# Kernel optimization log

Hardware: AMD Instinct MI355X
Metric: run time of the kernel (lower is better)

## Reference

```python
import jax, jax.numpy as jnp
import numpy as np

# dims
B, L, HID, TDIM, LT = 8, 4096, 1024, 768, 77
DIM = 512            # vmamba_dim
D_INNER = 2 * DIM    # expand = 2
NHEADS = DIM // 16   # 32
HEADDIM = D_INNER // NHEADS  # 32
D_STATE = 64
CONV_K = 4
CONV_DIM = D_INNER + 2 * D_STATE  # 1152
D_PROJ = 2 * D_INNER + 2 * D_STATE + NHEADS  # z | xBC | dt


def setup_inputs() -> dict:
    key = jax.random.key(0)
    ks = jax.random.split(key, 20)
    s = 0.02
    return {
        "image_tokens": jax.random.normal(ks[0], (B, L, HID), jnp.float32),
        "text_tokens": jax.random.normal(ks[1], (B, LT, TDIM), jnp.float32),
        "W_in": jax.random.normal(ks[2], (HID, DIM), jnp.float32) * s,
        "b_in": jnp.zeros((DIM,), jnp.float32),
        "W_txt": jax.random.normal(ks[3], (TDIM, DIM), jnp.float32) * s,
        "b_txt": jnp.zeros((DIM,), jnp.float32),
        "norm_w": jnp.ones((DIM,), jnp.float32),
        "norm_b": jnp.zeros((DIM,), jnp.float32),
        "W_zxbcdt": jax.random.normal(ks[4], (DIM, D_PROJ), jnp.float32) * s,
        "b_zxbcdt": jnp.zeros((D_PROJ,), jnp.float32),
        "conv_w": jax.random.normal(ks[5], (CONV_DIM, CONV_K), jnp.float32) * 0.1,
        "conv_b": jnp.zeros((CONV_DIM,), jnp.float32),
        "dt_bias": jax.random.uniform(ks[6], (NHEADS,), jnp.float32, -4.0, -2.0),
        "A_log": jnp.log(jnp.arange(1, NHEADS + 1, dtype=jnp.float32)),
        "D": jnp.ones((NHEADS,), jnp.float32),
        "W_blk_out": jax.random.normal(ks[7], (D_INNER, DIM), jnp.float32) * s,
        "b_blk_out": jnp.zeros((DIM,), jnp.float32),
        "W_out": jax.random.normal(ks[8], (DIM, HID), jnp.float32) * s,
        "b_out": jnp.zeros((HID,), jnp.float32),
    }


def _layernorm(x, w, b, eps=1e-5):
    mu = x.mean(-1, keepdims=True)
    var = ((x - mu) ** 2).mean(-1, keepdims=True)
    return (x - mu) * jax.lax.rsqrt(var + eps) * w + b


def _mamba2_block(tok, norm_w, norm_b, W_zxbcdt, b_zxbcdt, conv_w, conv_b,
                  dt_bias, A_log, Dp, W_blk_out, b_blk_out):
    x = _layernorm(tok, norm_w, norm_b)
    zxbcdt = x @ W_zxbcdt + b_zxbcdt                       # [B,L,D_PROJ]
    z = zxbcdt[..., :D_INNER]
    xBC = zxbcdt[..., D_INNER:D_INNER + CONV_DIM]
    dt = zxbcdt[..., D_INNER + CONV_DIM:]                  # [B,L,H]
    # causal depthwise conv1d, kernel 4
    xp = jnp.pad(xBC, ((0, 0), (CONV_K - 1, 0), (0, 0)))
    conv = sum(xp[:, k:k + L, :] * conv_w[None, None, :, k] for k in range(CONV_K))
    xBC = jax.nn.silu(conv + conv_b)
    xh = xBC[..., :D_INNER].reshape(B, L, NHEADS, HEADDIM)  # [B,L,H,P]
    Bm = xBC[..., D_INNER:D_INNER + D_STATE]                # [B,L,N]
    Cm = xBC[..., D_INNER + D_STATE:]                       # [B,L,N]
    dt = jax.nn.softplus(dt + dt_bias)                      # [B,L,H]
    A = -jnp.exp(A_log)                                     # [H]
    dA = jnp.exp(dt * A)                                    # [B,L,H]

    def step(h, xs):
        dA_t, dt_t, B_t, C_t, x_t = xs   # [B,H],[B,H],[B,N],[B,N],[B,H,P]
        h = h * dA_t[:, :, None, None] + \
            (dt_t[:, :, None, None] * x_t[..., None]) * B_t[:, None, None, :]
        y = jnp.einsum('bhpn,bn->bhp', h, C_t)
        return h, y

    xs = (dA.transpose(1, 0, 2), dt.transpose(1, 0, 2),
          Bm.transpose(1, 0, 2), Cm.transpose(1, 0, 2),
          xh.transpose(1, 0, 2, 3))
    h0 = jnp.zeros((B, NHEADS, HEADDIM, D_STATE), tok.dtype)
    _, ys = jax.lax.scan(step, h0, xs)                      # [L,B,H,P]
    y = ys.transpose(1, 0, 2, 3) + Dp[None, None, :, None] * xh
    y = y.reshape(B, L, D_INNER) * jax.nn.silu(z)
    return tok + (y @ W_blk_out + b_blk_out)                # residual


def reference(image_tokens, text_tokens, W_in, b_in, W_txt, b_txt,
              norm_w, norm_b, W_zxbcdt, b_zxbcdt, conv_w, conv_b,
              dt_bias, A_log, D, W_blk_out, b_blk_out, W_out, b_out):
    txt = text_tokens[:, 0, :] @ W_txt + b_txt              # cls pool
    tok = image_tokens @ W_in + b_in + txt[:, None, :]
    tok = _mamba2_block(tok, norm_w, norm_b, W_zxbcdt, b_zxbcdt, conv_w,
                        conv_b, dt_bias, A_log, D, W_blk_out, b_blk_out)
    tok = tok @ W_out + b_out                               # [B,L,HID]
    return tok.mean(axis=1)                                 # AdaptiveAvgPool1d(1)
```

## Files before the change

### kernel.cpp

```cpp
#include <hip/hip_runtime.h>

typedef unsigned short U16;
typedef __attribute__((ext_vector_type(2))) float f32x2;
typedef __attribute__((ext_vector_type(4))) float f32x4;
typedef __attribute__((ext_vector_type(8))) short short8;
typedef __attribute__((ext_vector_type(8))) __bf16 bf16x8;

#define Bsz 8
#define Lsz 4096
#define HID 1024
#define DIMV 512
#define D_INNER 1024
#define NHEADS 32
#define HEADDIM 32
#define D_STATE 64
#define CONV_DIM 1152
#define D_PROJ 2208
#define D_PROJ_PAD 2304
#define MROWS 32768
#define CL2 256
#define NSUB 4
#define NCH 16

__device__ __forceinline__ float bf2f(U16 u) {
  return __builtin_bit_cast(float, (unsigned)(((unsigned)u) << 16));
}
__device__ __forceinline__ U16 f2bf(float f) {
  unsigned u = __builtin_bit_cast(unsigned, f);
  return (U16)((u + 0x7FFFu + ((u >> 16) & 1u)) >> 16);
}
__device__ __forceinline__ void gload_lds16(const void* g, void* l) {
  __builtin_amdgcn_global_load_lds((const __attribute__((address_space(1))) unsigned int*)g,
                                   (__attribute__((address_space(3))) unsigned int*)l, 16, 0, 0);
}

__global__ __launch_bounds__(512) void txt_kernel(const float* __restrict__ text,
                                                  const float* __restrict__ Wt,
                                                  const float* __restrict__ bt,
                                                  float* __restrict__ txt) {
  int b = blockIdx.x, j = threadIdx.x;
  float s = bt[j];
  const float* tp = text + (size_t)b * 77 * 768;
  for (int k = 0; k < 768; ++k) s += tp[k] * Wt[(size_t)k * 512 + j];
  txt[b * 512 + j] = s;
}

__global__ __launch_bounds__(256) void transpose_cvt_kernel(const float* __restrict__ in,
                                                            U16* __restrict__ out,
                                                            int K, int N, int Npad) {
  __shared__ U16 tile[32][33];
  int n0 = blockIdx.x * 32, k0 = blockIdx.y * 32;
  int tx = threadIdx.x, ty = threadIdx.y;
  #pragma unroll
  for (int i = 0; i < 4; ++i) {
    int k = k0 + ty + i * 8, n = n0 + tx;
    float v = (n < N) ? in[(size_t)k * N + n] : 0.f;
    tile[ty + i * 8][tx] = f2bf(v);
  }
  __syncthreads();
  #pragma unroll
  for (int i = 0; i < 4; ++i) {
    int n = n0 + ty + i * 8;
    out[(size_t)n * K + k0 + tx] = tile[tx][ty + i * 8];
  }
}

template <int EPI, int AF32>
__global__ __launch_bounds__(256) void gemm_kernel(const void* __restrict__ Ap,
                                                   const U16* __restrict__ Bt,
                                                   U16* __restrict__ C,
                                                   const float* __restrict__ bias,
                                                   const float* __restrict__ txtv,
                                                   int M, int K, int Nreal) {
  __shared__ alignas(16) U16 As[128 * 64];
  __shared__ alignas(16) U16 Bs[128 * 64];
  const int tid = threadIdx.x;
  const int wid = tid >> 6, lane = tid & 63;
  const int lhi = lane >> 4, llo = lane & 15;
  const int m0 = blockIdx.x * 128;
  const int n0 = blockIdx.y * 128;
  const int wr = wid >> 1, wc = wid & 1;
  f32x4 acc[4][4] = {};

  for (int k0 = 0; k0 < K; k0 += 64) {
    __syncthreads();
    if constexpr (AF32) {
      const float* Af = (const float*)Ap;
      #pragma unroll
      for (int is = 0; is < 4; ++is) {
        int q = is * 256 + tid;
        int r = q >> 3, cl = q & 7;
        int cg = cl ^ (r & 7);
        const float* src = Af + (size_t)(m0 + r) * K + k0 + cg * 8;
        f32x4 v0 = *reinterpret_cast<const f32x4*>(src);
        f32x4 v1 = *reinterpret_cast<const f32x4*>(src + 4);
        short8 o;
        #pragma unroll
        for (int j = 0; j < 4; ++j) {
          o[j] = (short)f2bf(v0[j]);
          o[j + 4] = (short)f2bf(v1[j]);
        }
        *reinterpret_cast<short8*>(&As[q * 8]) = o;
      }
    } else {
      const U16* A = (const U16*)Ap;
      #pragma unroll
      for (int is = 0; is < 4; ++is) {
        int qbase = is * 256 + wid * 64;
        int q = qbase + lane;
        int r = q >> 3;
        int cc = (q & 7) ^ (r & 7);
        gload_lds16(A + (size_t)(m0 + r) * K + k0 + cc * 8, &As[qbase * 8]);
      }
    }
    #pragma unroll
    for (int is = 0; is < 4; ++is) {
      int qbase = is * 256 + wid * 64;
      int q = qbase + lane;
      int r = q >> 3;
      int cc = (q & 7) ^ (r & 7);
      gload_lds16(Bt + (size_t)(n0 + r) * K + k0 + cc * 8, &Bs[qbase * 8]);
    }
    __syncthreads();
    #pragma unroll
    for (int kk = 0; kk < 64; kk += 32) {
      bf16x8 av[4], bv[4];
      #pragma unroll
      for (int i = 0; i < 4; ++i) {
        int ra = wr * 64 + i * 16 + llo;
        short8 a = *reinterpret_cast<const short8*>(
            &As[ra * 64 + ((((kk >> 3) + lhi) ^ (ra & 7)) << 3)]);
        av[i] = __builtin_bit_cast(bf16x8, a);
        int rb = wc * 64 + i * 16 + llo;
        short8 b = *reinterpret_cast<const short8*>(
            &Bs[rb * 64 + ((((kk >> 3) + lhi) ^ (rb & 7)) << 3)]);
        bv[i] = __builtin_bit_cast(bf16x8, b);
      }
      #pragma unroll
      for (int i = 0; i < 4; ++i)
        #pragma unroll
        for (int j = 0; j < 4; ++j)
          acc[i][j] = __builtin_amdgcn_mfma_f32_16x16x32_bf16(av[i], bv[j], acc[i][j], 0, 0, 0);
    }
  }
  const int b = m0 >> 12;
  #pragma unroll
  for (int i = 0; i < 4; ++i) {
    int rbase = m0 + wr * 64 + i * 16 + lhi * 4;
    #pragma unroll
    for (int j = 0; j < 4; ++j) {
      int cg = n0 + wc * 64 + j * 16 + llo;
      if (cg < Nreal) {
        float badd = bias[cg] + (EPI ? txtv[b * 512 + cg] : 0.f);
        #pragma unroll
        for (int r = 0; r < 4; ++r)
          C[(size_t)(rbase + r) * Nreal + cg] = f2bf(acc[i][j][r] + badd);
      }
    }
  }
}

__global__ __launch_bounds__(128) void ln_kernel(const U16* __restrict__ tok,
                                                 U16* __restrict__ xo,
                                                 const float* __restrict__ w,
                                                 const float* __restrict__ bb) {
  int row = blockIdx.x, tid = threadIdx.x;
  const U16* rp = tok + (size_t)row * 512 + tid * 4;
  uint2 raw = *reinterpret_cast<const uint2*>(rp);
  float f0 = bf2f((U16)(raw.x & 0xffff)), f1 = bf2f((U16)(raw.x >> 16));
  float f2 = bf2f((U16)(raw.y & 0xffff)), f3 = bf2f((U16)(raw.y >> 16));
  float s = f0 + f1 + f2 + f3;
  float q = f0 * f0 + f1 * f1 + f2 * f2 + f3 * f3;
  for (int m = 1; m < 64; m <<= 1) { s += __shfl_xor(s, m); q += __shfl_xor(q, m); }
  __shared__ float ss[2], qq[2];
  if ((tid & 63) == 0) { ss[tid >> 6] = s; qq[tid >> 6] = q; }
  __syncthreads();
  s = ss[0] + ss[1]; q = qq[0] + qq[1];
  float mu = s * (1.f / 512.f);
  float var = q * (1.f / 512.f) - mu * mu;
  float rs = rsqrtf(var + 1e-5f);
  int j0 = tid * 4;
  unsigned c0 = f2bf((f0 - mu) * rs * w[j0] + bb[j0]);
  unsigned c1 = f2bf((f1 - mu) * rs * w[j0 + 1] + bb[j0 + 1]);
  unsigned c2 = f2bf((f2 - mu) * rs * w[j0 + 2] + bb[j0 + 2]);
  unsigned c3 = f2bf((f3 - mu) * rs * w[j0 + 3] + bb[j0 + 3]);
  uint2 o; o.x = c0 | (c1 << 16); o.y = c2 | (c3 << 16);
  *reinterpret_cast<uint2*>(xo + (size_t)row * 512 + j0) = o;
}

__global__ __launch_bounds__(256) void tokpart_kernel(const U16* __restrict__ tok,
                                                      float* __restrict__ part) {
  int b = blockIdx.x, j = blockIdx.y * 256 + threadIdx.x, z = blockIdx.z;
  float s = 0.f;
  int l0 = z * 256;
  for (int l = l0; l < l0 + 256; ++l)
    s += bf2f(tok[((size_t)b * Lsz + l) * 512 + j]);
  part[(z * 8 + b) * 512 + j] = s;
}

__global__ __launch_bounds__(256) void decay_kernel(const U16* __restrict__ zx,
                                                    const float* __restrict__ dt_bias,
                                                    const float* __restrict__ A_log,
                                                    float* __restrict__ decay4) {
  const int sc = blockIdx.x;
  const int w = threadIdx.x >> 6, l = threadIdx.x & 63;
  const int r0 = sc * 64;
  const int b = r0 >> 12, l0 = r0 & 4095;
  #pragma unroll
  for (int i = 0; i < 8; ++i) {
    int hh = w * 8 + i;
    float raw = bf2f(zx[(size_t)(r0 + l) * D_PROJ + 2176 + hh]) + dt_bias[hh];
    float dt = (raw > 20.f) ? raw : log1pf(__expf(raw));
    float A = -__expf(A_log[hh]);
    float ldA2 = dt * A * 1.44269504088896f;
    float ldt2 = __log2f(dt);
    float la = ldA2;
    #pragma unroll
    for (int d = 1; d < 64; d <<= 1) {
      float o = __shfl_up(la, d);
      if (l >= d) la += o;
    }
    float laend = __shfl(la, 63);
    f32x4 v = {ldt2 - la, la, exp2f(la), exp2f(laend + ldt2 - la)};
    *reinterpret_cast<f32x4*>(decay4 + ((size_t)(b * 32 + hh) * 4096 + l0 + l) * 4) = v;
  }
}

__global__ __launch_bounds__(256) void conv_tr_kernel(
    const U16* __restrict__ zx, const float* __restrict__ cw,
    const float* __restrict__ cb, U16* __restrict__ Bmo, U16* __restrict__ Cmo,
    U16* __restrict__ xh_t, U16* __restrict__ gz_t,
    U16* __restrict__ bm_t, U16* __restrict__ cm_t) {
  __shared__ U16 tile[64 * 72];
  const int lt = blockIdx.x, ct = blockIdx.y;
  const int r0 = lt * 64;
  const int b = r0 >> 12, l0 = r0 & 4095;
  const int tid = threadIdx.x;
  const int c = tid & 63, lqb = tid >> 6;

  if (ct < 16) {
    const int zc0 = ct * 64;
    #pragma unroll
    for (int it = 0; it < 4; ++it) {
      int lq4 = (lqb + it * 4) * 4;
      float v[4];
      #pragma unroll
      for (int j = 0; j < 4; ++j) {
        float z = bf2f(zx[(size_t)(r0 + lq4 + j) * D_PROJ + zc0 + c]);
        v[j] = z / (1.f + __expf(-z));
      }
      uint2 p2;
      p2.x = (unsigned)f2bf(v[0]) | ((unsigned)f2bf(v[1]) << 16);
      p2.y = (unsigned)f2bf(v[2]) | ((unsigned)f2bf(v[3]) << 16);
      *reinterpret_cast<uint2*>(reinterpret_cast<char*>(tile) + (size_t)c * 144 + lq4 * 2) = p2;
    }
    __syncthreads();
    int c2 = tid >> 2, seg = tid & 3;
    const char* src = reinterpret_cast<const char*>(tile) + (size_t)c2 * 144 + seg * 32;
    f32x4 a = *reinterpret_cast<const f32x4*>(src);
    f32x4 bq = *reinterpret_cast<const f32x4*>(src + 16);
    U16* dst = gz_t + ((size_t)b * 1024 + zc0 + c2) * 4096 + l0 + seg * 16;
    *reinterpret_cast<f32x4*>(dst) = a;
    *reinterpret_cast<f32x4*>(dst + 8) = bq;
  } else {
    const int cc = (ct - 16) * 64 + c;
    const float4 w4 = *reinterpret_cast<const float4*>(cw + cc * 4);
    const float cbv = cb[cc];
    #pragma unroll
    for (int it = 0; it < 4; ++it) {
      int lq4 = (lqb + it * 4) * 4;
      float v7[7];
      #pragma unroll
      for (int k = 0; k < 7; ++k) {
        int lrel = lq4 + k - 3;
        v7[k] = (l0 + lrel >= 0)
                    ? bf2f(zx[(size_t)(r0 + lrel) * D_PROJ + D_INNER + cc])
                    : 0.f;
      }
      float o[4];
      #pragma unroll
      for (int j = 0; j < 4; ++j) {
        float acc = cbv + v7[j] * w4.x + v7[j + 1] * w4.y + v7[j + 2] * w4.z + v7[j + 3] * w4.w;
        o[j] = acc / (1.f + __expf(-acc));
      }
      uint2 p2;
      p2.x = (unsigned)f2bf(o[0]) | ((unsigned)f2bf(o[1]) << 16);
      p2.y = (unsigned)f2bf(o[2]) | ((unsigned)f2bf(o[3]) << 16);
      *reinterpret_cast<uint2*>(reinterpret_cast<char*>(tile) + (size_t)c * 144 + lq4 * 2) = p2;
      if (cc >= 1024) {
        U16* outp = (cc < 1088) ? Bmo : Cmo;
        int n = cc & 63;
        #pragma unroll
        for (int j = 0; j < 4; ++j)
          outp[(size_t)(r0 + lq4 + j) * 64 + n] = f2bf(o[j]);
      }
    }
    __syncthreads();
    int c2 = tid >> 2, seg = tid & 3;
    const char* src = reinterpret_cast<const char*>(tile) + (size_t)c2 * 144 + seg * 32;
    f32x4 a = *reinterpret_cast<const f32x4*>(src);
    f32x4 bq = *reinterpret_cast<const f32x4*>(src + 16);
    int cc2 = (ct - 16) * 64 + c2;
    U16* dst;
    if (cc2 < 1024)      dst = xh_t + ((size_t)b * 1024 + cc2) * 4096 + l0 + seg * 16;
    else if (cc2 < 1088) dst = bm_t + ((size_t)(b * 64 + cc2 - 1024)) * 4096 + l0 + seg * 16;
    else                 dst = cm_t + ((size_t)(b * 64 + cc2 - 1088)) * 4096 + l0 + seg * 16;
    *reinterpret_cast<f32x4*>(dst) = a;
    *reinterpret_cast<f32x4*>(dst + 8) = bq;
  }
}

__global__ __launch_bounds__(256, 2) void scan_chunk_kernel(
    const U16* __restrict__ xh_t, const U16* __restrict__ gz_t,
    const U16* __restrict__ Bm, const U16* __restrict__ Cm,
    const U16* __restrict__ bm_t, const U16* __restrict__ cm_t,
    const float* __restrict__ decay4, const float* __restrict__ Dp,
    U16* __restrict__ hpart, U16* __restrict__ wacc,
    float* __restrict__ ylocal, float* __restrict__ aprod) {
  const int w = threadIdx.x >> 6, l = threadIdx.x & 63;
  const int bid = (blockIdx.x & 7) * 128 + (blockIdx.x >> 3);
  const int u = bid * 4 + w;
  const int hh = u & 31, ci = (u >> 5) & (NCH - 1), b = u >> 9;
  const int tl = l & 15, lg = l >> 4;

  __shared__ alignas(16) U16 MsmAll[4 * 64 * 72];
  __shared__ alignas(16) float decAll[4 * 256];
  U16* Msm = &MsmAll[w * 64 * 72];
  float* qsm = &decAll[w * 256];
  float* la2sm = qsm + 64;
  float* casm = qsm + 128;
  float* cfsm = qsm + 192;

  #pragma unroll
  for (int i = 0; i < 9; ++i)
    *reinterpret_cast<f32x4*>(reinterpret_cast<char*>(Msm) + (size_t)l * 144 + i * 16) =
        f32x4{0.f, 0.f, 0.f, 0.f};

  f32x4 hC[2][4] = {};
  f32x4 WB[2][4] = {};
  f32x4 corrp[2] = {};
  float ylac[2] = {0.f, 0.f}, dxac[2] = {0.f, 0.f};
  float capfx = 1.f;
  const size_t xgrow = ((size_t)b * 1024 + hh * 32) * 4096;
  const float* dbase = decay4 + ((size_t)(b * 32 + hh) * 4096) * 4;

  for (int sc = 0; sc < NSUB; ++sc) {
    const int lglob = ci * CL2 + sc * 64;
    const int r0g = b * 4096 + lglob;

    f32x4 dv = *reinterpret_cast<const f32x4*>(dbase + (size_t)(lglob + l) * 4);
    qsm[l] = dv[0];
    la2sm[l] = dv[1];
    casm[l] = dv[2];
    cfsm[l] = dv[3];
    const float cs = __shfl(dv[2], 63);

    {
      f32x4 g[7] = {};
      #pragma unroll
      for (int k = 0; k < 2; ++k) {
        bf16x8 af0 = *reinterpret_cast<const bf16x8*>(
            Bm + (size_t)(r0g + tl) * 64 + k * 32 + lg * 8);
        bf16x8 af1 = *reinterpret_cast<const bf16x8*>(
            Bm + (size_t)(r0g + 16 + tl) * 64 + k * 32 + lg * 8);
        #pragma unroll
        for (int ti = 0; ti < 4; ++ti) {
          bf16x8 cf = *reinterpret_cast<const bf16x8*>(
              Cm + (size_t)(r0g + ti * 16 + tl) * 64 + k * 32 + lg * 8);
          g[ti] = __builtin_amdgcn_mfma_f32_16x16x32_bf16(af0, cf, g[ti], 0, 0, 0);
          if (ti >= 1)
            g[3 + ti] = __builtin_amdgcn_mfma_f32_16x16x32_bf16(af1, cf, g[3 + ti], 0, 0, 0);
        }
      }
      f32x4 q0 = *reinterpret_cast<const f32x4*>(&qsm[lg * 4]);
      f32x4 q1 = *reinterpret_cast<const f32x4*>(&qsm[16 + lg * 4]);
      #pragma unroll
      for (int idx = 0; idx < 7; ++idx) {
        const int si = (idx < 4) ? 0 : 1;
        const int ti = (idx < 4) ? idx : (idx - 3);
        f32x4 q4 = si ? q1 : q0;
        float lat = la2sm[ti * 16 + tl];
        float v[4];
        #pragma unroll
        for (int r = 0; r < 4; ++r) {
          float val = g[idx][r] * exp2f(lat + q4[r]);
          if (si == ti) val = (lg * 4 + r <= tl) ? val : 0.f;
          v[r] = val;
        }
        uint2 pk;
        pk.x = (unsigned)f2bf(v[0]) | ((unsigned)f2bf(v[1]) << 16);
        pk.y = (unsigned)f2bf(v[2]) | ((unsigned)f2bf(v[3]) << 16);
        *reinterpret_cast<uint2*>(reinterpret_cast<char*>(Msm) +
                                  (size_t)(ti * 16 + tl) * 144 + (size_t)(si * 16 + lg * 4) * 2) = pk;
      }
    }
    {
      f32x4 g[3] = {};
      #pragma unroll
      for (int k = 0; k < 2; ++k) {
        bf16x8 af2 = *reinterpret_cast<const bf16x8*>(
            Bm + (size_t)(r0g + 32 + tl) * 64 + k * 32 + lg * 8);
        bf16x8 af3 = *reinterpret_cast<const bf16x8*>(
            Bm + (size_t)(r0g + 48 + tl) * 64 + k * 32 + lg * 8);
        bf16x8 cf2 = *reinterpret_cast<const bf16x8*>(
            Cm + (size_t)(r0g + 32 + tl) * 64 + k * 32 + lg * 8);
        bf16x8 cf3 = *reinterpret_cast<const bf16x8*>(
            Cm + (size_t)(r0g + 48 + tl) * 64 + k * 32 + lg * 8);
        g[0] = __builtin_amdgcn_mfma_f32_16x16x32_bf16(af2, cf2, g[0], 0, 0, 0);
        g[1] = __builtin_amdgcn_mfma_f32_16x16x32_bf16(af2, cf3, g[1], 0, 0, 0);
        g[2] = __builtin_amdgcn_mfma_f32_16x16x32_bf16(af3, cf3, g[2], 0, 0, 0);
      }
      f32x4 q2 = *reinterpret_cast<const f32x4*>(&qsm[32 + lg * 4]);
      f32x4 q3 = *reinterpret_cast<const f32x4*>(&qsm[48 + lg * 4]);
      const int sis[3] = {2, 2, 3};
      const int tis[3] = {2, 3, 3};
      #pragma unroll
      for (int idx = 0; idx < 3; ++idx) {
        const int si = sis[idx], ti = tis[idx];
        f32x4 q4 = (si == 2) ? q2 : q3;
        float lat = la2sm[ti * 16 + tl];
        float v[4];
        #pragma unroll
        for (int r = 0; r < 4; ++r) {
          float val = g[idx][r] * exp2f(lat + q4[r]);
          if (si == ti) val = (lg * 4 + r <= tl) ? val : 0.f;
          v[r] = val;
        }
        uint2 pk;
        pk.x = (unsigned)f2bf(v[0]) | ((unsigned)f2bf(v[1]) << 16);
        pk.y = (unsigned)f2bf(v[2]) | ((unsigned)f2bf(v[3]) << 16);
        *reinterpret_cast<uint2*>(reinterpret_cast<char*>(Msm) +
                                  (size_t)(ti * 16 + tl) * 144 + (size_t)(si * 16 + lg * 4) * 2) = pk;
      }
    }

    {
      bf16x8 xb[2][2];
      #pragma unroll
      for (int pt = 0; pt < 2; ++pt)
        #pragma unroll
        for (int ks = 0; ks < 2; ++ks)
          xb[pt][ks] = *reinterpret_cast<const bf16x8*>(
              xh_t + xgrow + (size_t)(pt * 16 + tl) * 4096 + lglob + ks * 32 + lg * 8);
      #pragma unroll
      for (int tt = 0; tt < 4; ++tt) {
        f32x4 y[2] = {f32x4{0.f, 0.f, 0.f, 0.f}, f32x4{0.f, 0.f, 0.f, 0.f}};
        #pragma unroll
        for (int ks = 0; ks < 2; ++ks) {
          bf16x8 mf = *reinterpret_cast<const bf16x8*>(
              reinterpret_cast<char*>(Msm) + (size_t)(tt * 16 + tl) * 144 + (ks * 32 + lg * 8) * 2);
          #pragma unroll
          for (int pt = 0; pt < 2; ++pt)
            y[pt] = __builtin_amdgcn_mfma_f32_16x16x32_bf16(mf, xb[pt][ks], y[pt], 0, 0, 0);
        }
        #pragma unroll
        for (int pt = 0; pt < 2; ++pt) {
          size_t ro = xgrow + (size_t)(pt * 16 + tl) * 4096 + lglob + tt * 16 + lg * 4;
          uint2 gz2 = *reinterpret_cast<const uint2*>(gz_t + ro);
          uint2 xx2 = *reinterpret_cast<const uint2*>(xh_t + ro);
          float gzv[4] = {bf2f((U16)(gz2.x & 0xffff)), bf2f((U16)(gz2.x >> 16)),
                          bf2f((U16)(gz2.y & 0xffff)), bf2f((U16)(gz2.y >> 16))};
          float xxv[4] = {bf2f((U16)(xx2.x & 0xffff)), bf2f((U16)(xx2.x >> 16)),
                          bf2f((U16)(xx2.y & 0xffff)), bf2f((U16)(xx2.y >> 16))};
          #pragma unroll
          for (int r = 0; r < 4; ++r) {
            ylac[pt] = fmaf(gzv[r], y[pt][r], ylac[pt]);
            dxac[pt] = fmaf(gzv[r], xxv[r], dxac[pt]);
          }
        }
      }
    }

    bf16x8 ga[2][2], xa[2][2];
    #pragma unroll
    for (int pt = 0; pt < 2; ++pt)
      #pragma unroll
      for (int kt = 0; kt < 2; ++kt) {
        size_t ro = xgrow + (size_t)(pt * 16 + tl) * 4096 + lglob + kt * 32 + lg * 8;
        short8 graw = *reinterpret_cast<const short8*>(gz_t + ro);
        short8 xraw = *reinterpret_cast<const short8*>(xh_t + ro);
        const float* cap = &casm[kt * 32 + lg * 8];
        const float* cfp = &cfsm[kt * 32 + lg * 8];
        short8 gs, xs8;
        #pragma unroll
        for (int j = 0; j < 8; ++j) {
          gs[j] = (short)f2bf(bf2f((U16)graw[j]) * cap[j]);
          xs8[j] = (short)f2bf(bf2f((U16)xraw[j]) * cfp[j]);
        }
        ga[pt][kt] = __builtin_bit_cast(bf16x8, gs);
        xa[pt][kt] = __builtin_bit_cast(bf16x8, xs8);
      }

    #pragma unroll
    for (int nt = 0; nt < 4; ++nt) {
      size_t cro = (size_t)(b * 64 + nt * 16 + tl) * 4096 + lglob;
      bf16x8 cb0 = *reinterpret_cast<const bf16x8*>(cm_t + cro + lg * 8);
      bf16x8 cb1 = *reinterpret_cast<const bf16x8*>(cm_t + cro + 32 + lg * 8);
      bf16x8 bb0 = *reinterpret_cast<const bf16x8*>(bm_t + cro + lg * 8);
      bf16x8 bb1 = *reinterpret_cast<const bf16x8*>(bm_t + cro + 32 + lg * 8);
      #pragma unroll
      for (int pt = 0; pt < 2; ++pt) {
        f32x4 z4 = {0.f, 0.f, 0.f, 0.f};
        f32x4 ws = __builtin_amdgcn_mfma_f32_16x16x32_bf16(ga[pt][0], cb0, z4, 0, 0, 0);
        ws = __builtin_amdgcn_mfma_f32_16x16x32_bf16(ga[pt][1], cb1, ws, 0, 0, 0);
        f32x4 hs = __builtin_amdgcn_mfma_f32_16x16x32_bf16(xa[pt][0], bb0, z4, 0, 0, 0);
        hs = __builtin_amdgcn_mfma_f32_16x16x32_bf16(xa[pt][1], bb1, hs, 0, 0, 0);
        corrp[pt] = corrp[pt] + hC[pt][nt] * ws;
        WB[pt][nt] = WB[pt][nt] + ws * capfx;
        hC[pt][nt] = hC[pt][nt] * cs + hs;
      }
    }
    capfx *= cs;
  }

  #pragma unroll
  for (int pt = 0; pt < 2; ++pt)
    #pragma unroll
    for (int nt = 0; nt < 4; ++nt) {
      size_t slot = (size_t)u * 2048 + (size_t)((pt * 4 + nt) * 64 + l) * 4;
      ushort4 hp, wp;
      hp.x = f2bf(hC[pt][nt][0]); hp.y = f2bf(hC[pt][nt][1]);
      hp.z = f2bf(hC[pt][nt][2]); hp.w = f2bf(hC[pt][nt][3]);
      wp.x = f2bf(WB[pt][nt][0]); wp.y = f2bf(WB[pt][nt][1]);
      wp.z = f2bf(WB[pt][nt][2]); wp.w = f2bf(WB[pt][nt][3]);
      *reinterpret_cast<ushort4*>(hpart + slot) = hp;
      *reinterpret_cast<ushort4*>(wacc + slot) = wp;
    }
  float corrv[2][4];
  #pragma unroll
  for (int pt = 0; pt < 2; ++pt)
    #pragma unroll
    for (int r = 0; r < 4; ++r) {
      float c = corrp[pt][r];
      c += __shfl_xor(c, 1); c += __shfl_xor(c, 2);
      c += __shfl_xor(c, 4); c += __shfl_xor(c, 8);
      corrv[pt][r] = c;
    }
  const float Dh = Dp[hh];
  float* ysm = qsm;
  #pragma unroll
  for (int pt = 0; pt < 2; ++pt) {
    float yv = ylac[pt] + Dh * dxac[pt];
    yv += __shfl_xor(yv, 16);
    yv += __shfl_xor(yv, 32);
    if (l < 16) ysm[pt * 16 + l] = yv;
  }
  if (tl == 0) {
    #pragma unroll
    for (int pt = 0; pt < 2; ++pt)
      #pragma unroll
      for (int r = 0; r < 4; ++r)
        ysm[pt * 16 + lg * 4 + r] += corrv[pt][r];
  }
  if (l < 32) ylocal[(size_t)u * 32 + l] = ysm[l];
  if (l == 0) aprod[u] = capfx;
}

__global__ __launch_bounds__(256) void scan_combine_kernel(
    const U16* __restrict__ hpart, const U16* __restrict__ wacc,
    const float* __restrict__ ylocal, const float* __restrict__ aprod,
    float* __restrict__ yysum) {
  const int bh = blockIdx.x;
  const int b = bh >> 5, hh = bh & 31;
  const int w = threadIdx.x >> 6, l = threadIdx.x & 63;
  const int tl = l & 15, lg = l >> 4;
  __shared__ float csm[8][16];
  __shared__ float ylsm[32];
  const int pair0 = w * 2;
  f32x4 hr[2] = {};
  float cv[2][4] = {};
  for (int ci = 0; ci < NCH; ++ci) {
    int bx = (b * NCH + ci) * 32 + hh;
    size_t base = (size_t)bx * 2048 + (size_t)l * 4;
    float ap = aprod[bx];
    #pragma unroll
    for (int k = 0; k < 2; ++k) {
      size_t o = base + (size_t)(pair0 + k) * 256;
      ushort4 wraw = *reinterpret_cast<const ushort4*>(wacc + o);
      ushort4 praw = *reinterpret_cast<const ushort4*>(hpart + o);
      f32x4 wv = {bf2f(wraw.x), bf2f(wraw.y), bf2f(wraw.z), bf2f(wraw.w)};
      f32x4 pv = {bf2f(praw.x), bf2f(praw.y), bf2f(praw.z), bf2f(praw.w)};
      f32x4 a4 = hr[k] * wv;
      #pragma unroll
      for (int r = 0; r < 4; ++r) cv[k][r] += a4[r];
      hr[k] = hr[k] * ap + pv;
    }
  }
  #pragma unroll
  for (int k = 0; k < 2; ++k)
    #pragma unroll
    for (int r = 0; r < 4; ++r) {
      float c = cv[k][r];
      c += __shfl_xor(c, 1); c += __shfl_xor(c, 2);
      c += __shfl_xor(c, 4); c += __shfl_xor(c, 8);
      if (tl == 0) csm[pair0 + k][lg * 4 + r] = c;
    }
  if (threadIdx.x < 32) {
    float yl = 0.f;
    for (int ci = 0; ci < NCH; ++ci)
      yl += ylocal[(size_t)((b * NCH + ci) * 32 + hh) * 32 + threadIdx.x];
    ylsm[threadIdx.x] = yl;
  }
  __syncthreads();
  if (threadIdx.x < 32) {
    int p = threadIdx.x;
    int pt = p >> 4, pl = p & 15;
    float corr = csm[pt * 4 + 0][pl] + csm[pt * 4 + 1][pl] +
                 csm[pt * 4 + 2][pl] + csm[pt * 4 + 3][pl];
    yysum[(size_t)b * 1024 + hh * 32 + p] = ylsm[p] + corr;
  }
}

__global__ __launch_bounds__(128) void final1_kernel(const float* __restrict__ tokpart,
                                                     const float* __restrict__ yysum,
                                                     const float* __restrict__ Wb,
                                                     const float* __restrict__ bb,
                                                     float* __restrict__ m2) {
  int b = blockIdx.x, j = blockIdx.y * 128 + threadIdx.x;
  float tm = 0.f;
  #pragma unroll
  for (int z = 0; z < 16; ++z) tm += tokpart[(z * 8 + b) * 512 + j];
  float s = 0.f;
  for (int d = 0; d < 1024; ++d) s += yysum[b * 1024 + d] * Wb[(size_t)d * 512 + j];
  m2[b * 512 + j] = (tm + s) * (1.f / (float)Lsz) + bb[j];
}

__global__ __launch_bounds__(256) void final2_kernel(const float* __restrict__ m2,
                                                     const float* __restrict__ Wo,
                                                     const float* __restrict__ bo,
                                                     float* __restrict__ out) {
  int b = blockIdx.x, o = blockIdx.y * 256 + threadIdx.x;
  float s = 0.f;
  for (int j = 0; j < 512; ++j) s += m2[b * 512 + j] * Wo[(size_t)j * 1024 + o];
  out[b * 1024 + o] = s + bo[o];
}

extern "C" void kernel_launch(void* const* d_in, const int* in_sizes, int n_in,
                              void* d_out, int out_size, void* d_ws, size_t ws_size,
                              hipStream_t stream) {
  const float* image = (const float*)d_in[0];
  const float* text = (const float*)d_in[1];
  const float* W_in = (const float*)d_in[2];
  const float* b_in = (const float*)d_in[3];
  const float* W_txt = (const float*)d_in[4];
  const float* b_txt = (const float*)d_in[5];
  const float* norm_w = (const float*)d_in[6];
  const float* norm_b = (const float*)d_in[7];
  const float* W_zx = (const float*)d_in[8];
  const float* b_zx = (const float*)d_in[9];
  const float* conv_w = (const float*)d_in[10];
  const float* conv_b = (const float*)d_in[11];
  const float* dt_bias = (const float*)d_in[12];
  const float* A_log = (const float*)d_in[13];
  const float* Dp = (const float*)d_in[14];
  const float* W_blk = (const float*)d_in[15];
  const float* b_blk = (const float*)d_in[16];
  const float* W_out = (const float*)d_in[17];
  const float* b_out = (const float*)d_in[18];
  float* out = (float*)d_out;

  char* ws = (char*)d_ws;
  size_t off = 0;
  auto take = [&](size_t bytes) {
    char* p = ws + off;
    off = (off + bytes + 255) & ~(size_t)255;
    return p;
  };
  U16* gz_t = (U16*)take((size_t)MROWS * HID * 2);
  U16* wt_in = (U16*)take((size_t)DIMV * HID * 2);
  U16* wt_zx = (U16*)take((size_t)D_PROJ_PAD * DIMV * 2);
  U16* tok_bf = (U16*)take((size_t)MROWS * DIMV * 2);
  U16* x_bf = (U16*)take((size_t)MROWS * DIMV * 2);
  U16* zx_bf = (U16*)take((size_t)MROWS * D_PROJ * 2);
  U16* xh_t = (U16*)take((size_t)MROWS * D_INNER * 2);
  U16* bm_bf = (U16*)take((size_t)MROWS * 64 * 2);
  U16* cm_bf = (U16*)take((size_t)MROWS * 64 * 2);
  U16* bm_t = (U16*)take((size_t)MROWS * 64 * 2);
  U16* cm_t = (U16*)take((size_t)MROWS * 64 * 2);
  float* decay4 = (float*)take((size_t)256 * 4096 * 16);
  float* txtf = (float*)take(8 * 512 * 4);
  float* tokpart = (float*)take(16 * 8 * 512 * 4);
  float* yysum = (float*)take(8 * 1024 * 4);
  float* m2 = (float*)take(8 * 512 * 4);
  float* ylocal = (float*)take((size_t)4096 * 32 * 4);
  float* aprod = (float*)take((size_t)4096 * 4);
  U16* hpart = tok_bf;
  U16* wacc = x_bf;

  txt_kernel<<<8, 512, 0, stream>>>(text, W_txt, b_txt, txtf);
  transpose_cvt_kernel<<<dim3(DIMV / 32, HID / 32), dim3(32, 8), 0, stream>>>(W_in, wt_in, HID, DIMV, DIMV);
  transpose_cvt_kernel<<<dim3(D_PROJ_PAD / 32, DIMV / 32), dim3(32, 8), 0, stream>>>(W_zx, wt_zx, DIMV, D_PROJ, D_PROJ_PAD);

  gemm_kernel<1, 1><<<dim3(MROWS / 128, DIMV / 128), 256, 0, stream>>>(
      (const void*)image, wt_in, tok_bf, b_in, txtf, MROWS, HID, DIMV);
  tokpart_kernel<<<dim3(8, 2, 16), 256, 0, stream>>>(tok_bf, tokpart);
  ln_kernel<<<MROWS, 128, 0, stream>>>(tok_bf, x_bf, norm_w, norm_b);

  gemm_kernel<0, 0><<<dim3(MROWS / 128, D_PROJ_PAD / 128), 256, 0, stream>>>(
      (const void*)x_bf, wt_zx, zx_bf, b_zx, nullptr, MROWS, DIMV, D_PROJ);

  decay_kernel<<<512, 256, 0, stream>>>(zx_bf, dt_bias, A_log, decay4);
  conv_tr_kernel<<<dim3(MROWS / 64, 34), 256, 0, stream>>>(zx_bf, conv_w, conv_b, bm_bf, cm_bf,
                                                           xh_t, gz_t, bm_t, cm_t);

  scan_chunk_kernel<<<1024, 256, 0, stream>>>(xh_t, gz_t, bm_bf, cm_bf, bm_t, cm_t,
                                              decay4, Dp, hpart, wacc, ylocal, aprod);
  scan_combine_kernel<<<256, 256, 0, stream>>>(hpart, wacc, ylocal, aprod, yysum);

  final1_kernel<<<dim3(8, 4), 128, 0, stream>>>(tokpart, yysum, W_blk, b_blk, m2);
  final2_kernel<<<dim3(8, 4), 256, 0, stream>>>(m2, W_out, b_out, out);
}
```

Before: 612.3 us.

## Emit transposed zxbcdt from in_proj GEMM with fused SiLU gate

The in_proj GEMM epilogue now transposes its tile through shared memory and writes zxbcdt in a channel-major [B, D_PROJ_PAD, L] layout, applying SiLU to the z columns inline. The separate gz_t buffer and row-major zx buffer go away. The conv kernel is rewritten to read contiguous time rows per channel, with each thread computing 64 outputs, and it re-transposes B and C for the row-major copies. The aim is to remove the strided row-major reads and the extra transpose pass, at the cost of a heavier GEMM epilogue and more registers per thread in the conv kernel.

```diff
diff --git a/kernel.cpp b/kernel.cpp
--- a/kernel.cpp
+++ b/kernel.cpp
@@ -1,7 +1,6 @@
 #include <hip/hip_runtime.h>
 
 typedef unsigned short U16;
-typedef __attribute__((ext_vector_type(2))) float f32x2;
 typedef __attribute__((ext_vector_type(4))) float f32x4;
 typedef __attribute__((ext_vector_type(8))) short short8;
 typedef __attribute__((ext_vector_type(8))) __bf16 bf16x8;
@@ -65,15 +64,16 @@
   }
 }
 
-template <int EPI, int AF32>
+template <int EPI, int AF32, int TRANS>
 __global__ __launch_bounds__(256) void gemm_kernel(const void* __restrict__ Ap,
                                                    const U16* __restrict__ Bt,
                                                    U16* __restrict__ C,
                                                    const float* __restrict__ bias,
                                                    const float* __restrict__ txtv,
                                                    int M, int K, int Nreal) {
-  __shared__ alignas(16) U16 As[128 * 64];
-  __shared__ alignas(16) U16 Bs[128 * 64];
+  __shared__ alignas(16) U16 smem[128 * 128];
+  U16* As = smem;
+  U16* Bs = smem + 128 * 64;
   const int tid = threadIdx.x;
   const int wid = tid >> 6, lane = tid & 63;
   const int lhi = lane >> 4, llo = lane & 15;
@@ -144,17 +144,61 @@
     }
   }
   const int b = m0 >> 12;
-  #pragma unroll
-  for (int i = 0; i < 4; ++i) {
-    int rbase = m0 + wr * 64 + i * 16 + lhi * 4;
-    #pragma unroll
-    for (int j = 0; j < 4; ++j) {
-      int cg = n0 + wc * 64 + j * 16 + llo;
-      if (cg < Nreal) {
-        float badd = bias[cg] + (EPI ? txtv[b * 512 + cg] : 0.f);
-        #pragma unroll
-        for (int r = 0; r < 4; ++r)
-          C[(size_t)(rbase + r) * Nreal + cg] = f2bf(acc[i][j][r] + badd);
+  if constexpr (TRANS) {
+    __syncthreads();
+    U16* T = smem;
+    #pragma unroll
+    for (int i = 0; i < 4; ++i) {
+      #pragma unroll
+      for (int j = 0; j < 4; ++j) {
+        int c_loc = wc * 64 + j * 16 + llo;
+        int cg = n0 + c_loc;
+        float badd = (cg < D_PROJ) ? bias[cg] : 0.f;
+        int q = wr * 16 + i * 4 + lhi;
+        int qs = q ^ ((c_loc & 15) << 1);
+        U16 pk[4];
+        #pragma unroll
+        for (int r = 0; r < 4; ++r) {
+          float v = acc[i][j][r] + badd;
+          if (cg < 1024) v = v / (1.f + __expf(-v));
+          pk[r] = f2bf(v);
+        }
+        uint2 p2;
+        p2.x = (unsigned)pk[0] | ((unsigned)pk[1] << 16);
+        p2.y = (unsigned)pk[2] | ((unsigned)pk[3] << 16);
+        *reinterpret_cast<uint2*>(&T[c_loc * 128 + qs * 4]) = p2;
+      }
+    }
+    __syncthreads();
+    const int l0 = m0 & 4095;
+    #pragma unroll
+    for (int cs = 0; cs < 8; ++cs) {
+      int c = cs * 16 + (tid >> 4);
+      int gch = n0 + c;
+      int kp = (tid & 15) * 2;
+      int q0 = kp ^ ((c & 15) << 1);
+      int q1 = (kp + 1) ^ ((c & 15) << 1);
+      uint2 a = *reinterpret_cast<const uint2*>(&T[c * 128 + q0 * 4]);
+      uint2 bq = *reinterpret_cast<const uint2*>(&T[c * 128 + q1 * 4]);
+      if (gch < D_PROJ) {
+        uint4 oo;
+        oo.x = a.x; oo.y = a.y; oo.z = bq.x; oo.w = bq.y;
+        *reinterpret_cast<uint4*>(C + ((size_t)b * D_PROJ_PAD + gch) * 4096 + l0 + kp * 4) = oo;
+      }
+    }
+  } else {
+    #pragma unroll
+    for (int i = 0; i < 4; ++i) {
+      int rbase = m0 + wr * 64 + i * 16 + lhi * 4;
+      #pragma unroll
+      for (int j = 0; j < 4; ++j) {
+        int cg = n0 + wc * 64 + j * 16 + llo;
+        if (cg < Nreal) {
+          float badd = bias[cg] + (EPI ? txtv[b * 512 + cg] : 0.f);
+          #pragma unroll
+          for (int r = 0; r < 4; ++r)
+            C[(size_t)(rbase + r) * Nreal + cg] = f2bf(acc[i][j][r] + badd);
+        }
       }
     }
   }
@@ -198,7 +242,7 @@
   part[(z * 8 + b) * 512 + j] = s;
 }
 
-__global__ __launch_bounds__(256) void decay_kernel(const U16* __restrict__ zx,
+__global__ __launch_bounds__(256) void decay_kernel(const U16* __restrict__ zxT,
                                                     const float* __restrict__ dt_bias,
                                                     const float* __restrict__ A_log,
                                                     float* __restrict__ decay4) {
@@ -209,7 +253,7 @@
   #pragma unroll
   for (int i = 0; i < 8; ++i) {
     int hh = w * 8 + i;
-    float raw = bf2f(zx[(size_t)(r0 + l) * D_PROJ + 2176 + hh]) + dt_bias[hh];
+    float raw = bf2f(zxT[((size_t)b * D_PROJ_PAD + 2176 + hh) * 4096 + l0 + l]) + dt_bias[hh];
     float dt = (raw > 20.f) ? raw : log1pf(__expf(raw));
     float A = -__expf(A_log[hh]);
     float ldA2 = dt * A * 1.44269504088896f;
@@ -226,92 +270,91 @@
   }
 }
 
-__global__ __launch_bounds__(256) void conv_tr_kernel(
-    const U16* __restrict__ zx, const float* __restrict__ cw,
-    const float* __restrict__ cb, U16* __restrict__ Bmo, U16* __restrict__ Cmo,
-    U16* __restrict__ xh_t, U16* __restrict__ gz_t,
-    U16* __restrict__ bm_t, U16* __restrict__ cm_t) {
-  __shared__ U16 tile[64 * 72];
-  const int lt = blockIdx.x, ct = blockIdx.y;
-  const int r0 = lt * 64;
-  const int b = r0 >> 12, l0 = r0 & 4095;
+__global__ __launch_bounds__(256) void conv_t_kernel(
+    const U16* __restrict__ zxT, const float* __restrict__ cw,
+    const float* __restrict__ cb, U16* __restrict__ xh_t,
+    U16* __restrict__ bm_t, U16* __restrict__ cm_t,
+    U16* __restrict__ Bmo, U16* __restrict__ Cmo) {
+  __shared__ U16 Tc[64 * 264];
+  const int lc = blockIdx.x, cg = blockIdx.y, b = blockIdx.z;
   const int tid = threadIdx.x;
-  const int c = tid & 63, lqb = tid >> 6;
-
-  if (ct < 16) {
-    const int zc0 = ct * 64;
-    #pragma unroll
-    for (int it = 0; it < 4; ++it) {
-      int lq4 = (lqb + it * 4) * 4;
-      float v[4];
-      #pragma unroll
-      for (int j = 0; j < 4; ++j) {
-        float z = bf2f(zx[(size_t)(r0 + lq4 + j) * D_PROJ + zc0 + c]);
-        v[j] = z / (1.f + __expf(-z));
-      }
-      uint2 p2;
-      p2.x = (unsigned)f2bf(v[0]) | ((unsigned)f2bf(v[1]) << 16);
-      p2.y = (unsigned)f2bf(v[2]) | ((unsigned)f2bf(v[3]) << 16);
-      *reinterpret_cast<uint2*>(reinterpret_cast<char*>(tile) + (size_t)c * 144 + lq4 * 2) = p2;
+  const int cl = tid & 63, ls = tid >> 6;
+  const int cc2 = cg * 64 + cl;
+  const int l0 = lc * 256 + ls * 64;
+  const U16* row = zxT + ((size_t)b * D_PROJ_PAD + 1024 + cc2) * 4096;
+
+  U16 arr[72];
+  {
+    const U16* src = row + l0 - 8;
+    #pragma unroll
+    for (int k = 0; k < 9; ++k) {
+      uint4 rv;
+      if (l0 == 0 && k == 0) {
+        rv.x = rv.y = rv.z = rv.w = 0u;
+      } else {
+        rv = *reinterpret_cast<const uint4*>(src + k * 8);
+      }
+      arr[k * 8 + 0] = (U16)(rv.x & 0xffff); arr[k * 8 + 1] = (U16)(rv.x >> 16);
+      arr[k * 8 + 2] = (U16)(rv.y & 0xffff); arr[k * 8 + 3] = (U16)(rv.y >> 16);
+      arr[k * 8 + 4] = (U16)(rv.z & 0xffff); arr[k * 8 + 5] = (U16)(rv.z >> 16);
+      arr[k * 8 + 6] = (U16)(rv.w & 0xffff); arr[k * 8 + 7] = (U16)(rv.w >> 16);
+    }
+  }
+  const float4 w4 = *reinterpret_cast<const float4*>(cw + cc2 * 4);
+  const float cbv = cb[cc2];
+  U16 o[64];
+  #pragma unroll
+  for (int j = 0; j < 64; ++j) {
+    float acc = cbv + bf2f(arr[j + 5]) * w4.x + bf2f(arr[j + 6]) * w4.y +
+                bf2f(arr[j + 7]) * w4.z + bf2f(arr[j + 8]) * w4.w;
+    o[j] = f2bf(acc / (1.f + __expf(-acc)));
+  }
+  {
+    U16* dst;
+    if (cc2 < 1024)      dst = xh_t + ((size_t)b * 1024 + cc2) * 4096 + l0;
+    else if (cc2 < 1088) dst = bm_t + ((size_t)(b * 64 + (cc2 - 1024))) * 4096 + l0;
+    else                 dst = cm_t + ((size_t)(b * 64 + (cc2 - 1088))) * 4096 + l0;
+    #pragma unroll
+    for (int k = 0; k < 8; ++k) {
+      uint4 ov;
+      ov.x = (unsigned)o[k * 8 + 0] | ((unsigned)o[k * 8 + 1] << 16);
+      ov.y = (unsigned)o[k * 8 + 2] | ((unsigned)o[k * 8 + 3] << 16);
+      ov.z = (unsigned)o[k * 8 + 4] | ((unsigned)o[k * 8 + 5] << 16);
+      ov.w = (unsigned)o[k * 8 + 6] | ((unsigned)o[k * 8 + 7] << 16);
+      *reinterpret_cast<uint4*>(dst + k * 8) = ov;
+    }
+  }
+  if (cg >= 16) {
+    #pragma unroll
+    for (int k = 0; k < 8; ++k) {
+      uint4 ov;
+      ov.x = (unsigned)o[k * 8 + 0] | ((unsigned)o[k * 8 + 1] << 16);
+      ov.y = (unsigned)o[k * 8 + 2] | ((unsigned)o[k * 8 + 3] << 16);
+      ov.z = (unsigned)o[k * 8 + 4] | ((unsigned)o[k * 8 + 5] << 16);
+      ov.w = (unsigned)o[k * 8 + 6] | ((unsigned)o[k * 8 + 7] << 16);
+      *reinterpret_cast<uint4*>(&Tc[cl * 264 + ls * 64 + k * 8]) = ov;
     }
     __syncthreads();
-    int c2 = tid >> 2, seg = tid & 3;
-    const char* src = reinterpret_cast<const char*>(tile) + (size_t)c2 * 144 + seg * 32;
-    f32x4 a = *reinterpret_cast<const f32x4*>(src);
-    f32x4 bq = *reinterpret_cast<const f32x4*>(src + 16);
-    U16* dst = gz_t + ((size_t)b * 1024 + zc0 + c2) * 4096 + l0 + seg * 16;
-    *reinterpret_cast<f32x4*>(dst) = a;
-    *reinterpret_cast<f32x4*>(dst + 8) = bq;
-  } else {
-    const int cc = (ct - 16) * 64 + c;
-    const float4 w4 = *reinterpret_cast<const float4*>(cw + cc * 4);
-    const float cbv = cb[cc];
-    #pragma unroll
-    for (int it = 0; it < 4; ++it) {
-      int lq4 = (lqb + it * 4) * 4;
-      float v7[7];
-      #pragma unroll
-      for (int k = 0; k < 7; ++k) {
-        int lrel = lq4 + k - 3;
-        v7[k] = (l0 + lrel >= 0)
-                    ? bf2f(zx[(size_t)(r0 + lrel) * D_PROJ + D_INNER + cc])
-                    : 0.f;
-      }
-      float o[4];
-      #pragma unroll
-      for (int j = 0; j < 4; ++j) {
-        float acc = cbv + v7[j] * w4.x + v7[j + 1] * w4.y + v7[j + 2] * w4.z + v7[j + 3] * w4.w;
-        o[j] = acc / (1.f + __expf(-acc));
-      }
-      uint2 p2;
-      p2.x = (unsigned)f2bf(o[0]) | ((unsigned)f2bf(o[1]) << 16);
-      p2.y = (unsigned)f2bf(o[2]) | ((unsigned)f2bf(o[3]) << 16);
-      *reinterpret_cast<uint2*>(reinterpret_cast<char*>(tile) + (size_t)c * 144 + lq4 * 2) = p2;
-      if (cc >= 1024) {
-        U16* outp = (cc < 1088) ? Bmo : Cmo;
-        int n = cc & 63;
-        #pragma unroll
-        for (int j = 0; j < 4; ++j)
-          outp[(size_t)(r0 + lq4 + j) * 64 + n] = f2bf(o[j]);
-      }
-    }
-    __syncthreads();
-    int c2 = tid >> 2, seg = tid & 3;
-    const char* src = reinterpret_cast<const char*>(tile) + (size_t)c2 * 144 + seg * 32;
-    f32x4 a = *reinterpret_cast<const f32x4*>(src);
-    f32x4 bq = *reinterpret_cast<const f32x4*>(src + 16);
-    int cc2 = (ct - 16) * 64 + c2;
-    U16* dst;
-    if (cc2 < 1024)      dst = xh_t + ((size_t)b * 1024 + cc2) * 4096 + l0 + seg * 16;
-    else if (cc2 < 1088) dst = bm_t + ((size_t)(b * 64 + cc2 - 1024)) * 4096 + l0 + seg * 16;
-    else                 dst = cm_t + ((size_t)(b * 64 + cc2 - 1088)) * 4096 + l0 + seg * 16;
-    *reinterpret_cast<f32x4*>(dst) = a;
-    *reinterpret_cast<f32x4*>(dst + 8) = bq;
+    U16* outp = (cg == 16) ? Bmo : Cmo;
+    const int lt = tid;
+    U16 rowv[64];
+    #pragma unroll
+    for (int n = 0; n < 64; ++n) rowv[n] = Tc[n * 264 + lt];
+    U16* dst = outp + ((size_t)b * 4096 + lc * 256 + lt) * 64;
+    #pragma unroll
+    for (int k = 0; k < 8; ++k) {
+      uint4 ov;
+      ov.x = (unsigned)rowv[k * 8 + 0] | ((unsigned)rowv[k * 8 + 1] << 16);
+      ov.y = (unsigned)rowv[k * 8 + 2] | ((unsigned)rowv[k * 8 + 3] << 16);
+      ov.z = (unsigned)rowv[k * 8 + 4] | ((unsigned)rowv[k * 8 + 5] << 16);
+      ov.w = (unsigned)rowv[k * 8 + 6] | ((unsigned)rowv[k * 8 + 7] << 16);
+      *reinterpret_cast<uint4*>(dst + k * 8) = ov;
+    }
   }
 }
 
 __global__ __launch_bounds__(256, 2) void scan_chunk_kernel(
-    const U16* __restrict__ xh_t, const U16* __restrict__ gz_t,
+    const U16* __restrict__ xh_t, const U16* __restrict__ zxT,
     const U16* __restrict__ Bm, const U16* __restrict__ Cm,
     const U16* __restrict__ bm_t, const U16* __restrict__ cm_t,
     const float* __restrict__ decay4, const float* __restrict__ Dp,
@@ -341,7 +384,8 @@
   f32x4 corrp[2] = {};
   float ylac[2] = {0.f, 0.f}, dxac[2] = {0.f, 0.f};
   float capfx = 1.f;
-  const size_t xgrow = ((size_t)b * 1024 + hh * 32) * 4096;
+  const size_t xrow = ((size_t)b * 1024 + hh * 32) * 4096;
+  const size_t grow = ((size_t)b * D_PROJ_PAD + hh * 32) * 4096;
   const float* dbase = decay4 + ((size_t)(b * 32 + hh) * 4096) * 4;
 
   for (int sc = 0; sc < NSUB; ++sc) {
@@ -441,7 +485,7 @@
         #pragma unroll
         for (int ks = 0; ks < 2; ++ks)
           xb[pt][ks] = *reinterpret_cast<const bf16x8*>(
-              xh_t + xgrow + (size_t)(pt * 16 + tl) * 4096 + lglob + ks * 32 + lg * 8);
+              xh_t + xrow + (size_t)(pt * 16 + tl) * 4096 + lglob + ks * 32 + lg * 8);
       #pragma unroll
       for (int tt = 0; tt < 4; ++tt) {
         f32x4 y[2] = {f32x4{0.f, 0.f, 0.f, 0.f}, f32x4{0.f, 0.f, 0.f, 0.f}};
@@ -455,9 +499,9 @@
         }
         #pragma unroll
         for (int pt = 0; pt < 2; ++pt) {
-          size_t ro = xgrow + (size_t)(pt * 16 + tl) * 4096 + lglob + tt * 16 + lg * 4;
-          uint2 gz2 = *reinterpret_cast<const uint2*>(gz_t + ro);
-          uint2 xx2 = *reinterpret_cast<const uint2*>(xh_t + ro);
+          size_t po = (size_t)(pt * 16 + tl) * 4096 + lglob + tt * 16 + lg * 4;
+          uint2 gz2 = *reinterpret_cast<const uint2*>(zxT + grow + po);
+          uint2 xx2 = *reinterpret_cast<const uint2*>(xh_t + xrow + po);
           float gzv[4] = {bf2f((U16)(gz2.x & 0xffff)), bf2f((U16)(gz2.x >> 16)),
                           bf2f((U16)(gz2.y & 0xffff)), bf2f((U16)(gz2.y >> 16))};
           float xxv[4] = {bf2f((U16)(xx2.x & 0xffff)), bf2f((U16)(xx2.x >> 16)),
@@ -476,9 +520,9 @@
     for (int pt = 0; pt < 2; ++pt)
       #pragma unroll
       for (int kt = 0; kt < 2; ++kt) {
-        size_t ro = xgrow + (size_t)(pt * 16 + tl) * 4096 + lglob + kt * 32 + lg * 8;
-        short8 graw = *reinterpret_cast<const short8*>(gz_t + ro);
-        short8 xraw = *reinterpret_cast<const short8*>(xh_t + ro);
+        size_t po = (size_t)(pt * 16 + tl) * 4096 + lglob + kt * 32 + lg * 8;
+        short8 graw = *reinterpret_cast<const short8*>(zxT + grow + po);
+        short8 xraw = *reinterpret_cast<const short8*>(xh_t + xrow + po);
         const float* cap = &casm[kt * 32 + lg * 8];
         const float* cfp = &cfsm[kt * 32 + lg * 8];
         short8 gs, xs8;
@@ -666,12 +710,11 @@
     off = (off + bytes + 255) & ~(size_t)255;
     return p;
   };
-  U16* gz_t = (U16*)take((size_t)MROWS * HID * 2);
+  U16* zxT = (U16*)take((size_t)Bsz * D_PROJ_PAD * 4096 * 2);
   U16* wt_in = (U16*)take((size_t)DIMV * HID * 2);
   U16* wt_zx = (U16*)take((size_t)D_PROJ_PAD * DIMV * 2);
   U16* tok_bf = (U16*)take((size_t)MROWS * DIMV * 2);
   U16* x_bf = (U16*)take((size_t)MROWS * DIMV * 2);
-  U16* zx_bf = (U16*)take((size_t)MROWS * D_PROJ * 2);
   U16* xh_t = (U16*)take((size_t)MROWS * D_INNER * 2);
   U16* bm_bf = (U16*)take((size_t)MROWS * 64 * 2);
   U16* cm_bf = (U16*)take((size_t)MROWS * 64 * 2);
@@ -691,19 +734,19 @@
   transpose_cvt_kernel<<<dim3(DIMV / 32, HID / 32), dim3(32, 8), 0, stream>>>(W_in, wt_in, HID, DIMV, DIMV);
   transpose_cvt_kernel<<<dim3(D_PROJ_PAD / 32, DIMV / 32), dim3(32, 8), 0, stream>>>(W_zx, wt_zx, DIMV, D_PROJ, D_PROJ_PAD);
 
-  gemm_kernel<1, 1><<<dim3(MROWS / 128, DIMV / 128), 256, 0, stream>>>(
+  gemm_kernel<1, 1, 0><<<dim3(MROWS / 128, DIMV / 128), 256, 0, stream>>>(
       (const void*)image, wt_in, tok_bf, b_in, txtf, MROWS, HID, DIMV);
   tokpart_kernel<<<dim3(8, 2, 16), 256, 0, stream>>>(tok_bf, tokpart);
   ln_kernel<<<MROWS, 128, 0, stream>>>(tok_bf, x_bf, norm_w, norm_b);
 
-  gemm_kernel<0, 0><<<dim3(MROWS / 128, D_PROJ_PAD / 128), 256, 0, stream>>>(
-      (const void*)x_bf, wt_zx, zx_bf, b_zx, nullptr, MROWS, DIMV, D_PROJ);
-
-  decay_kernel<<<512, 256, 0, stream>>>(zx_bf, dt_bias, A_log, decay4);
-  conv_tr_kernel<<<dim3(MROWS / 64, 34), 256, 0, stream>>>(zx_bf, conv_w, conv_b, bm_bf, cm_bf,
-                                                           xh_t, gz_t, bm_t, cm_t);
-
-  scan_chunk_kernel<<<1024, 256, 0, stream>>>(xh_t, gz_t, bm_bf, cm_bf, bm_t, cm_t,
+  gemm_kernel<0, 0, 1><<<dim3(MROWS / 128, D_PROJ_PAD / 128), 256, 0, stream>>>(
+      (const void*)x_bf, wt_zx, zxT, b_zx, nullptr, MROWS, DIMV, D_PROJ);
+
+  decay_kernel<<<512, 256, 0, stream>>>(zxT, dt_bias, A_log, decay4);
+  conv_t_kernel<<<dim3(16, 18, 8), 256, 0, stream>>>(zxT, conv_w, conv_b,
+                                                     xh_t, bm_t, cm_t, bm_bf, cm_bf);
+
+  scan_chunk_kernel<<<1024, 256, 0, stream>>>(xh_t, zxT, bm_bf, cm_bf, bm_t, cm_t,
                                               decay4, Dp, hpart, wacc, ylocal, aprod);
   scan_combine_kernel<<<256, 256, 0, stream>>>(hpart, wacc, ylocal, aprod, yysum);
 
```

Result: faster. 580.0 us (-5.3%).
